# Kernel optimization log

Measured on AMD Instinct MI355X. Metric: run time of the kernel, lower is better.

## Reference

```python
import jax, jax.numpy as jnp
import numpy as np

B, S, DM = 2, 2048, 2048
H, DH = 16, 128
EPS = 1e-6


def rmsnorm(t, w):
    # normalize over last dim (head_dim), fp32 math
    var = jnp.mean(jnp.square(t), axis=-1, keepdims=True)
    return t * jax.lax.rsqrt(var + EPS) * w


def apply_rope(t, freqs):
    # t: (B,S,H,D); freqs: (S,1,D/2,2,2)
    b, s, h, d = t.shape
    t2 = t.reshape(b, s, h, 2, d // 2)
    t2 = jnp.moveaxis(t2, -2, -1)[..., None, :]  # (B,S,H,D/2,1,2)
    out = freqs[..., 0] * t2[..., 0] + freqs[..., 1] * t2[..., 1]  # (B,S,H,D/2,2)
    out = jnp.moveaxis(out, -1, -2).reshape(b, s, h, d)
    return out.astype(t.dtype)


def setup_inputs() -> dict:
    key = jax.random.key(0)
    ks = jax.random.split(key, 6)
    sc = 0.02
    return {
        "x": jax.random.normal(ks[0], (B, S, DM), jnp.float32),
        "rope_emb": jax.random.normal(ks[1], (S, 1, DH // 2, 2, 2), jnp.float32),
        "wq": jax.random.normal(ks[2], (DM, DM), jnp.float32) * sc,
        "wk": jax.random.normal(ks[3], (DM, DM), jnp.float32) * sc,
        "wv": jax.random.normal(ks[4], (DM, DM), jnp.float32) * sc,
        "wo": jax.random.normal(ks[5], (DM, DM), jnp.float32) * sc,
        "q_norm_w": jnp.ones((DH,), jnp.float32),
        "k_norm_w": jnp.ones((DH,), jnp.float32),
    }


def reference(x, rope_emb, wq, wk, wv, wo, q_norm_w, k_norm_w):
    b, s, _ = x.shape
    q = (x @ wq.T).reshape(b, s, H, DH)
    k = (x @ wk.T).reshape(b, s, H, DH)
    v = (x @ wv.T).reshape(b, s, H, DH)
    q = rmsnorm(q, q_norm_w)
    k = rmsnorm(k, k_norm_w)
    q = apply_rope(q, rope_emb)
    k = apply_rope(k, rope_emb)
    scale = 1.0 / np.sqrt(DH).astype(np.float32)
    scores = jnp.einsum('bqhd,bkhd->bhqk', q, k) * scale
    attn = jax.nn.softmax(scores, axis=-1)
    out = jnp.einsum('bhqk,bkhd->bqhd', attn, v).reshape(b, s, H * DH)
    return out @ wo.T
```

## Files before the change

kernel.cpp:

```cpp
#include <hip/hip_runtime.h>

typedef __bf16 bf16x8 __attribute__((ext_vector_type(8)));
typedef __bf16 bf16x4 __attribute__((ext_vector_type(4)));
typedef float floatx4 __attribute__((ext_vector_type(4)));

#define GK 2048
#define S_LEN 2048
#define NH 16
#define DH 128
#define NKT (GK / 64)

__device__ __forceinline__ void gl2lds16c(const __bf16* g, char* l) {
    __builtin_amdgcn_global_load_lds(
        (const __attribute__((address_space(1))) void*)g,
        (__attribute__((address_space(3))) void*)l, 16, 0, 0);
}

__global__ __launch_bounds__(256) void cvt_bf16(const float* __restrict__ in,
                                                __bf16* __restrict__ out, int n4) {
    int i = blockIdx.x * 256 + threadIdx.x;
    if (i < n4) {
        const float4 v = ((const float4*)in)[i];
        bf16x4 h;
        h[0] = (__bf16)v.x; h[1] = (__bf16)v.y; h[2] = (__bf16)v.z; h[3] = (__bf16)v.w;
        ((bf16x4*)out)[i] = h;
    }
}

__global__ __launch_bounds__(256) void cvt3_bf16(const float* __restrict__ a,
                                                 const float* __restrict__ b,
                                                 const float* __restrict__ c,
                                                 __bf16* __restrict__ out) {
    const int per = 2048 * 2048 / 4;
    int i = blockIdx.x * 256 + threadIdx.x;
    const float* src = a; int j = i;
    if (i >= 2 * per)      { src = c; j = i - 2 * per; }
    else if (i >= per)     { src = b; j = i - per; }
    const float4 v = ((const float4*)src)[j];
    bf16x4 h;
    h[0] = (__bf16)v.x; h[1] = (__bf16)v.y; h[2] = (__bf16)v.z; h[3] = (__bf16)v.w;
    ((bf16x4*)out)[i] = h;
}

__device__ __forceinline__ int xcd_remap(int L, int nwg) {
    return (L & 7) * (nwg >> 3) + (L >> 3);
}

__device__ __forceinline__ void gemm_body3(const __bf16* __restrict__ A,
                                           const __bf16* __restrict__ W,
                                           int m0, int n0, char* lds,
                                           floatx4 (*acc)[4]) {
    const int t = threadIdx.x, l = t & 63, wave = t >> 6;
    const int fr = l & 15, fq = l >> 4;
    const int wm = wave >> 2, wn = wave & 3;

    const int swcol = ((l & 7) * 8) ^ (((l >> 3) & 7) * 8);
    const __bf16* gA = A + (size_t)(m0 + wave * 8 + (l >> 3)) * GK + swcol;
    const __bf16* gW = W + (size_t)(n0 + wave * 8 + (l >> 3)) * GK + swcol;
    char* const ldsW = lds + wave * 1024;

    auto stageA = [&](int p, int kt, int q) {
        gl2lds16c(gA + (size_t)q * 64 * GK + kt * 64,
                  ldsW + p * 65536 + q * 8192);
    };
    auto stageBh = [&](int p, int kt, int h) {
        gl2lds16c(gW + (size_t)h * 64 * GK + kt * 64,
                  ldsW + p * 65536 + 32768 + h * 8192);
    };

#pragma unroll
    for (int q = 0; q < 4; q++) stageA(0, 0, q);
#pragma unroll
    for (int h = 0; h < 4; h++) stageBh(0, 0, h);
#pragma unroll
    for (int q = 0; q < 4; q++) stageA(1, 1, q);
#pragma unroll
    for (int h = 0; h < 4; h++) stageBh(1, 1, h);

    const int sw = (fr & 7) << 4;
    const int cb0 = (fq * 16) ^ sw;
    const int cb1 = (64 + fq * 16) ^ sw;

    for (int t0 = 0; t0 < NKT; t0++) {
        const int p = t0 & 1;
        if (t0 == NKT - 1) { asm volatile("s_waitcnt vmcnt(0)" ::: "memory"); }
        else               { asm volatile("s_waitcnt vmcnt(8)" ::: "memory"); }
        __builtin_amdgcn_s_barrier();
        asm volatile("" ::: "memory");

        const char* bufA = lds + p * 65536;
        const char* bufB = bufA + 32768;

        bf16x8 bB[4][2];
#pragma unroll
        for (int j = 0; j < 4; j++) {
            const char* rb = bufB + (wn * 64 + j * 16 + fr) * 128;
            bB[j][0] = *(const bf16x8*)(rb + cb0);
            bB[j][1] = *(const bf16x8*)(rb + cb1);
        }

#pragma unroll
        for (int q = 0; q < 4; q++) {
            if (t0 + 2 < NKT) {
                if (q == 1) { stageA(p, t0 + 2, 0); stageBh(p, t0 + 2, 0); stageBh(p, t0 + 2, 1); }
                if (q == 2) { stageA(p, t0 + 2, 1); stageBh(p, t0 + 2, 2); stageBh(p, t0 + 2, 3); }
                if (q == 3) { stageA(p, t0 + 2, 2); }
            }
            const char* ra = bufA + (q * 64 + wm * 32 + fr) * 128;
            bf16x8 bA[2][2];
#pragma unroll
            for (int i = 0; i < 2; i++) {
                bA[i][0] = *(const bf16x8*)(ra + i * 2048 + cb0);
                bA[i][1] = *(const bf16x8*)(ra + i * 2048 + cb1);
            }
            __builtin_amdgcn_s_setprio(1);
#pragma unroll
            for (int i = 0; i < 2; i++)
#pragma unroll
                for (int j = 0; j < 4; j++) {
                    acc[2 * q + i][j] = __builtin_amdgcn_mfma_f32_16x16x32_bf16(bA[i][0], bB[j][0], acc[2 * q + i][j], 0, 0, 0);
                    acc[2 * q + i][j] = __builtin_amdgcn_mfma_f32_16x16x32_bf16(bA[i][1], bB[j][1], acc[2 * q + i][j], 0, 0, 0);
                }
            __builtin_amdgcn_s_setprio(0);
            __builtin_amdgcn_s_barrier();
            asm volatile("" ::: "memory");
        }
        if (t0 + 2 < NKT) stageA(p, t0 + 2, 3);
    }
}

__global__ __launch_bounds__(512, 2) void gemm_qkv(const __bf16* __restrict__ A,
                                                   const __bf16* __restrict__ W,
                                                   __bf16* __restrict__ qb,
                                                   __bf16* __restrict__ kb,
                                                   __bf16* __restrict__ vbT) {
    extern __shared__ __align__(16) char lds[];
    const int gx = gridDim.x;
    const int L = blockIdx.x + gx * blockIdx.y;
    const int tid2 = xcd_remap(L, gx * (int)gridDim.y);
    const int m0 = (tid2 / gx) * 256, n0 = (tid2 % gx) * 256;
    floatx4 acc[8][4] = {};
    gemm_body3(A, W, m0, n0, lds, acc);

    const int lane = threadIdx.x & 63, wave = threadIdx.x >> 6;
    const int fr = lane & 15, fq = lane >> 4;
    const int wm = wave >> 2, wn = wave & 3;
    const int which = n0 >> 11;
    const int nc0 = n0 & 2047;

    for (int mi = 0; mi < 8; mi++)
        for (int j = 0; j < 4; j++) {
            const int row = m0 + (mi >> 1) * 64 + wm * 32 + (mi & 1) * 16 + fq * 4;
            const int col = nc0 + wn * 64 + j * 16 + fr;
            if (which == 2) {
                __bf16* Cp = vbT + (((size_t)(row & ~2047)) << 11) +
                             (size_t)col * 2048 + (row & 2047);
                bf16x4 hv;
                for (int r = 0; r < 4; r++) hv[r] = (__bf16)acc[mi][j][r];
                *(bf16x4*)Cp = hv;
            } else {
                __bf16* dst = which ? kb : qb;
                for (int r = 0; r < 4; r++)
                    dst[(size_t)(row + r) * 2048 + col] = (__bf16)acc[mi][j][r];
            }
        }
}

__global__ __launch_bounds__(512, 2) void gemm_out(const __bf16* __restrict__ A,
                                                   const __bf16* __restrict__ W,
                                                   float* __restrict__ C) {
    extern __shared__ __align__(16) char lds[];
    const int gx = gridDim.x;
    const int L = blockIdx.x + gx * blockIdx.y;
    const int tid2 = xcd_remap(L, gx * (int)gridDim.y);
    const int m0 = (tid2 / gx) * 256, n0 = (tid2 % gx) * 256;
    floatx4 acc[8][4] = {};
    gemm_body3(A, W, m0, n0, lds, acc);

    const int lane = threadIdx.x & 63, wave = threadIdx.x >> 6;
    const int fr = lane & 15, fq = lane >> 4;
    const int wm = wave >> 2, wn = wave & 3;
    for (int mi = 0; mi < 8; mi++)
        for (int j = 0; j < 4; j++) {
            const int row = m0 + (mi >> 1) * 64 + wm * 32 + (mi & 1) * 16 + fq * 4;
            const int col = n0 + wn * 64 + j * 16 + fr;
            for (int r = 0; r < 4; r++)
                C[(size_t)(row + r) * 2048 + col] = acc[mi][j][r];
        }
}

__global__ __launch_bounds__(256) void rmsrope(__bf16* __restrict__ qb,
                                               __bf16* __restrict__ kb,
                                               const float* __restrict__ rope,
                                               const float* __restrict__ qw,
                                               const float* __restrict__ kw) {
    const int lane = threadIdx.x & 63;
    const int row = blockIdx.x * 4 + (threadIdx.x >> 6);
    __bf16* p = (blockIdx.y ? kb : qb) + (size_t)row * DH;
    const float* w = blockIdx.y ? kw : qw;
    const int s = (row >> 4) & (S_LEN - 1);

    float t0 = (float)p[lane];
    float t1 = (float)p[lane + 64];
    float ss = t0 * t0 + t1 * t1;
    for (int o = 32; o; o >>= 1) ss += __shfl_xor(ss, o, 64);
    const float inv = rsqrtf(ss * (1.0f / 128.0f) + 1e-6f);
    t0 *= inv * w[lane];
    t1 *= inv * w[lane + 64];

    const float4 f = *(const float4*)(rope + (size_t)s * 256 + lane * 4);
    p[lane]      = (__bf16)(f.x * t0 + f.y * t1);
    p[lane + 64] = (__bf16)(f.z * t0 + f.w * t1);
}

__global__ __launch_bounds__(256, 2) void flash(const __bf16* __restrict__ Q,
                                                const __bf16* __restrict__ K,
                                                const __bf16* __restrict__ Vt_g,
                                                __bf16* __restrict__ O) {
    extern __shared__ __align__(16) char lds[];

    const int t = threadIdx.x, lane = t & 63, wave = t >> 6;
    const int fr = lane & 15, fq = lane >> 4;

    const int n = blockIdx.x + (int)gridDim.x * blockIdx.y;
    const int by = (n & 7) * 4 + (n >> 7);
    const int bx = (n >> 3) & 15;
    const int b = by >> 4, h = by & 15;

    const size_t baseQ = (size_t)b * S_LEN * 2048 + h * 128;
    const size_t baseV = (size_t)b * 2048 * 2048 + (size_t)h * 128 * 2048;
    const int q0 = bx * 128 + wave * 32;
    const float sc2 = 0.08838834764831845f * 1.4426950408889634f;
    const float M2 = 12.0f * 1.4426950408889634f;

    bf16x8 qf[2][4];
#pragma unroll
    for (int i2 = 0; i2 < 2; i2++) {
        const __bf16* qp = Q + baseQ + (size_t)(q0 + i2 * 16 + fr) * 2048 + fq * 8;
#pragma unroll
        for (int c = 0; c < 4; c++) qf[i2][c] = *(const bf16x8*)(qp + c * 32);
    }
    asm volatile("s_waitcnt vmcnt(0)" ::: "memory");

    bf16x8 onesb;
#pragma unroll
    for (int e = 0; e < 8; e++) onesb[e] = (__bf16)1.0f;

    const int l4 = lane >> 4;
    const int c16 = lane & 15;
    const int l3 = lane >> 3;
    const int c8 = lane & 7;
    const __bf16* gK0 = K + baseQ + (size_t)(wave * 16 + l4) * 2048 + (c16 ^ l4) * 8;
    const __bf16* gK1 = K + baseQ + (size_t)(wave * 16 + l4) * 2048 + (c16 ^ (4 + l4)) * 8;
    const __bf16* gV  = Vt_g + baseV + (size_t)(wave * 8 + l3) * 2048 + (c8 ^ l3) * 8;

    char* const kdw = lds + wave * 4096;
    char* const vdw = lds + 32768 + wave * 1024;

    auto stage = [&](int p, int it2) {
        const size_t ko = (size_t)it2 * 64 * 2048;
        char* kd = kdw + p * 16384;
        gl2lds16c(gK0 + ko,                      kd);
        gl2lds16c(gK1 + ko + (size_t)4 * 2048,   kd + 1024);
        gl2lds16c(gK0 + ko + (size_t)8 * 2048,   kd + 2048);
        gl2lds16c(gK1 + ko + (size_t)12 * 2048,  kd + 3072);
        const __bf16* v = gV + it2 * 64;
        char* vd = vdw + p * 16384;
        gl2lds16c(v,                        vd);
        gl2lds16c(v + (size_t)32 * 2048,    vd + 4096);
        gl2lds16c(v + (size_t)64 * 2048,    vd + 8192);
        gl2lds16c(v + (size_t)96 * 2048,    vd + 12288);
    };

    stage(0, 0);
    stage(1, 1);

    floatx4 oa[2][9] = {};
    char* const Pw = lds + 65536 + wave * 4096;
    const int sw = (fr & 7) << 4;

    for (int it = 0; it < 32; ++it) {
        const int p = it & 1;
        if (it == 31) { asm volatile("s_waitcnt vmcnt(0)" ::: "memory"); }
        else          { asm volatile("s_waitcnt vmcnt(8)" ::: "memory"); }
        __builtin_amdgcn_s_barrier();
        asm volatile("" ::: "memory");

        const char* Kb = lds + p * 16384;
        const char* Vb = lds + 32768 + p * 16384;

        floatx4 sacc[2][4] = {};
#pragma unroll
        for (int j = 0; j < 4; j++) {
            const char* kr = Kb + (j * 16 + fr) * 256;
            const bf16x8 kf0 = *(const bf16x8*)(kr + ((0 + fq * 16) ^ sw));
            const bf16x8 kf1 = *(const bf16x8*)(kr + ((64 + fq * 16) ^ sw));
            const bf16x8 kf2 = *(const bf16x8*)(kr + ((128 + fq * 16) ^ sw));
            const bf16x8 kf3 = *(const bf16x8*)(kr + ((192 + fq * 16) ^ sw));
            __builtin_amdgcn_s_setprio(1);
            sacc[0][j] = __builtin_amdgcn_mfma_f32_16x16x32_bf16(qf[0][0], kf0, sacc[0][j], 0, 0, 0);
            sacc[1][j] = __builtin_amdgcn_mfma_f32_16x16x32_bf16(qf[1][0], kf0, sacc[1][j], 0, 0, 0);
            sacc[0][j] = __builtin_amdgcn_mfma_f32_16x16x32_bf16(qf[0][1], kf1, sacc[0][j], 0, 0, 0);
            sacc[1][j] = __builtin_amdgcn_mfma_f32_16x16x32_bf16(qf[1][1], kf1, sacc[1][j], 0, 0, 0);
            sacc[0][j] = __builtin_amdgcn_mfma_f32_16x16x32_bf16(qf[0][2], kf2, sacc[0][j], 0, 0, 0);
            sacc[1][j] = __builtin_amdgcn_mfma_f32_16x16x32_bf16(qf[1][2], kf2, sacc[1][j], 0, 0, 0);
            sacc[0][j] = __builtin_amdgcn_mfma_f32_16x16x32_bf16(qf[0][3], kf3, sacc[0][j], 0, 0, 0);
            sacc[1][j] = __builtin_amdgcn_mfma_f32_16x16x32_bf16(qf[1][3], kf3, sacc[1][j], 0, 0, 0);
            __builtin_amdgcn_s_setprio(0);
        }

#pragma unroll
        for (int i2 = 0; i2 < 2; i2++)
#pragma unroll
            for (int r = 0; r < 4; r++) {
                const int row = i2 * 16 + fq * 4 + r;
                char* pr = Pw + row * 128;
                const int rsw = ((fq * 4 + r) & 7) << 4;
#pragma unroll
                for (int j = 0; j < 4; j++)
                    *(__bf16*)(pr + ((j * 32 + fr * 2) ^ rsw)) =
                        (__bf16)exp2f(fmaf(sc2, sacc[i2][j][r], -M2));
            }

        bf16x8 pf[2][2];
#pragma unroll
        for (int i2 = 0; i2 < 2; i2++) {
            const char* pr = Pw + (i2 * 16 + fr) * 128;
            pf[i2][0] = *(const bf16x8*)(pr + ((fq * 16) ^ sw));
            pf[i2][1] = *(const bf16x8*)(pr + ((64 + fq * 16) ^ sw));
        }
#pragma unroll
        for (int nb = 0; nb < 8; nb++) {
            const char* vr = Vb + (nb * 16 + fr) * 128;
            const bf16x8 vf0 = *(const bf16x8*)(vr + ((fq * 16) ^ sw));
            const bf16x8 vf1 = *(const bf16x8*)(vr + ((64 + fq * 16) ^ sw));
            __builtin_amdgcn_s_setprio(1);
            oa[0][nb] = __builtin_amdgcn_mfma_f32_16x16x32_bf16(pf[0][0], vf0, oa[0][nb], 0, 0, 0);
            oa[1][nb] = __builtin_amdgcn_mfma_f32_16x16x32_bf16(pf[1][0], vf0, oa[1][nb], 0, 0, 0);
            oa[0][nb] = __builtin_amdgcn_mfma_f32_16x16x32_bf16(pf[0][1], vf1, oa[0][nb], 0, 0, 0);
            oa[1][nb] = __builtin_amdgcn_mfma_f32_16x16x32_bf16(pf[1][1], vf1, oa[1][nb], 0, 0, 0);
            __builtin_amdgcn_s_setprio(0);
        }
        oa[0][8] = __builtin_amdgcn_mfma_f32_16x16x32_bf16(pf[0][0], onesb, oa[0][8], 0, 0, 0);
        oa[1][8] = __builtin_amdgcn_mfma_f32_16x16x32_bf16(pf[1][0], onesb, oa[1][8], 0, 0, 0);
        oa[0][8] = __builtin_amdgcn_mfma_f32_16x16x32_bf16(pf[0][1], onesb, oa[0][8], 0, 0, 0);
        oa[1][8] = __builtin_amdgcn_mfma_f32_16x16x32_bf16(pf[1][1], onesb, oa[1][8], 0, 0, 0);

        __builtin_amdgcn_s_barrier();
        asm volatile("" ::: "memory");
        if (it < 30) stage(p, it + 2);
    }

    for (int i2 = 0; i2 < 2; i2++)
        for (int r = 0; r < 4; r++) {
            const float inv = 1.0f / oa[i2][8][r];
            __bf16* op = O + baseQ + (size_t)(q0 + i2 * 16 + fq * 4 + r) * 2048;
            for (int nb = 0; nb < 8; nb++)
                op[nb * 16 + fr] = (__bf16)(oa[i2][nb][r] * inv);
        }
}

extern "C" void kernel_launch(void* const* d_in, const int* in_sizes, int n_in,
                              void* d_out, int out_size, void* d_ws, size_t ws_size,
                              hipStream_t stream) {
    const float* x    = (const float*)d_in[0];
    const float* rope = (const float*)d_in[1];
    const float* wq   = (const float*)d_in[2];
    const float* wk   = (const float*)d_in[3];
    const float* wv   = (const float*)d_in[4];
    const float* wo   = (const float*)d_in[5];
    const float* qnw  = (const float*)d_in[6];
    const float* knw  = (const float*)d_in[7];
    float* out = (float*)d_out;

    static bool attr_set = false;
    if (!attr_set) {
        hipFuncSetAttribute((const void*)gemm_qkv,
                            hipFuncAttributeMaxDynamicSharedMemorySize, 131072);
        hipFuncSetAttribute((const void*)gemm_out,
                            hipFuncAttributeMaxDynamicSharedMemorySize, 131072);
        hipFuncSetAttribute((const void*)flash,
                            hipFuncAttributeMaxDynamicSharedMemorySize, 81920);
        attr_set = true;
    }

    const size_t NTOK = 2 * 2048;
    const size_t ELEMS = NTOK * 2048;
    __bf16* xb  = (__bf16*)d_ws;
    __bf16* qb  = xb + ELEMS;
    __bf16* kb  = qb + ELEMS;
    __bf16* vbT = kb + ELEMS;
    __bf16* ob  = xb;
    __bf16* wqkv = (__bf16*)d_out;
    __bf16* wob  = qb;

    cvt_bf16<<<(int)(ELEMS / 4) / 256, 256, 0, stream>>>(x, xb, (int)(ELEMS / 4));
    cvt3_bf16<<<3 * (2048 * 2048 / 4) / 256, 256, 0, stream>>>(wq, wk, wv, wqkv);
    gemm_qkv<<<dim3(6144 / 256, (unsigned)(NTOK / 256)), 512, 131072, stream>>>(xb, wqkv, qb, kb, vbT);
    rmsrope<<<dim3((unsigned)(NTOK * 16 / 4), 2), 256, 0, stream>>>(qb, kb, rope, qnw, knw);
    flash<<<dim3(S_LEN / 128, 2 * 16), 256, 81920, stream>>>(qb, kb, vbT, ob);
    cvt_bf16<<<(int)(2048 * 2048 / 4) / 256, 256, 0, stream>>>(wo, wob, 2048 * 2048 / 4);
    gemm_out<<<dim3(2048 / 256, (unsigned)(NTOK / 256)), 512, 131072, stream>>>(ob, wob, out);
}
```

Before: 411.2 us.

## Shrink GEMM M-tile to 128 and double-buffer A fragments in registers

Both GEMMs now use 128x256 tiles instead of 256x256. This halves the A-stage LDS footprint (96KB instead of 128KB) and the accumulator registers, and doubles the grid size. The fix is meant for poor wave/CU fill: the out-projection launched only 128 blocks and the QKV GEMM 384 blocks. The inner loop prefetches the next A fragment from LDS before issuing the current MFMAs, and the async-copy schedule and wait counts are adjusted to match. The cost is lower arithmetic intensity per tile and more global traffic for the W operand.

After: 406.6 us. About the same (-1.1%).

```diff
diff --git a/kernel.cpp b/kernel.cpp
--- a/kernel.cpp
+++ b/kernel.cpp
@@ -46,7 +46,7 @@
     return (L & 7) * (nwg >> 3) + (L >> 3);
 }
 
-__device__ __forceinline__ void gemm_body3(const __bf16* __restrict__ A,
+__device__ __forceinline__ void gemm_body4(const __bf16* __restrict__ A,
                                            const __bf16* __restrict__ W,
                                            int m0, int n0, char* lds,
                                            floatx4 (*acc)[4]) {
@@ -59,21 +59,19 @@
     const __bf16* gW = W + (size_t)(n0 + wave * 8 + (l >> 3)) * GK + swcol;
     char* const ldsW = lds + wave * 1024;
 
-    auto stageA = [&](int p, int kt, int q) {
-        gl2lds16c(gA + (size_t)q * 64 * GK + kt * 64,
-                  ldsW + p * 65536 + q * 8192);
+    auto stageA = [&](int p, int kt, int c) {
+        gl2lds16c(gA + (size_t)c * 64 * GK + kt * 64,
+                  ldsW + p * 49152 + c * 8192);
     };
     auto stageBh = [&](int p, int kt, int h) {
         gl2lds16c(gW + (size_t)h * 64 * GK + kt * 64,
-                  ldsW + p * 65536 + 32768 + h * 8192);
+                  ldsW + p * 49152 + 16384 + h * 8192);
     };
 
-#pragma unroll
-    for (int q = 0; q < 4; q++) stageA(0, 0, q);
+    stageA(0, 0, 0); stageA(0, 0, 1);
 #pragma unroll
     for (int h = 0; h < 4; h++) stageBh(0, 0, h);
-#pragma unroll
-    for (int q = 0; q < 4; q++) stageA(1, 1, q);
+    stageA(1, 1, 0); stageA(1, 1, 1);
 #pragma unroll
     for (int h = 0; h < 4; h++) stageBh(1, 1, h);
 
@@ -84,12 +82,12 @@
     for (int t0 = 0; t0 < NKT; t0++) {
         const int p = t0 & 1;
         if (t0 == NKT - 1) { asm volatile("s_waitcnt vmcnt(0)" ::: "memory"); }
-        else               { asm volatile("s_waitcnt vmcnt(8)" ::: "memory"); }
+        else               { asm volatile("s_waitcnt vmcnt(6)" ::: "memory"); }
         __builtin_amdgcn_s_barrier();
         asm volatile("" ::: "memory");
 
-        const char* bufA = lds + p * 65536;
-        const char* bufB = bufA + 32768;
+        const char* bufA = lds + p * 49152;
+        const char* bufB = bufA + 16384;
 
         bf16x8 bB[4][2];
 #pragma unroll
@@ -98,34 +96,35 @@
             bB[j][0] = *(const bf16x8*)(rb + cb0);
             bB[j][1] = *(const bf16x8*)(rb + cb1);
         }
+        bf16x8 af[2][2];
+        {
+            const char* ra = bufA + (wm * 16 + fr) * 128;
+            af[0][0] = *(const bf16x8*)(ra + cb0);
+            af[0][1] = *(const bf16x8*)(ra + cb1);
+        }
 
 #pragma unroll
         for (int q = 0; q < 4; q++) {
             if (t0 + 2 < NKT) {
-                if (q == 1) { stageA(p, t0 + 2, 0); stageBh(p, t0 + 2, 0); stageBh(p, t0 + 2, 1); }
-                if (q == 2) { stageA(p, t0 + 2, 1); stageBh(p, t0 + 2, 2); stageBh(p, t0 + 2, 3); }
-                if (q == 3) { stageA(p, t0 + 2, 2); }
+                if (q == 1) { stageBh(p, t0 + 2, 0); stageBh(p, t0 + 2, 1); }
+                if (q == 2) { stageBh(p, t0 + 2, 2); stageBh(p, t0 + 2, 3); stageA(p, t0 + 2, 0); }
             }
-            const char* ra = bufA + (q * 64 + wm * 32 + fr) * 128;
-            bf16x8 bA[2][2];
-#pragma unroll
-            for (int i = 0; i < 2; i++) {
-                bA[i][0] = *(const bf16x8*)(ra + i * 2048 + cb0);
-                bA[i][1] = *(const bf16x8*)(ra + i * 2048 + cb1);
+            if (q < 3) {
+                const char* ra = bufA + ((q + 1) * 32 + wm * 16 + fr) * 128;
+                af[(q + 1) & 1][0] = *(const bf16x8*)(ra + cb0);
+                af[(q + 1) & 1][1] = *(const bf16x8*)(ra + cb1);
             }
             __builtin_amdgcn_s_setprio(1);
 #pragma unroll
-            for (int i = 0; i < 2; i++)
-#pragma unroll
-                for (int j = 0; j < 4; j++) {
-                    acc[2 * q + i][j] = __builtin_amdgcn_mfma_f32_16x16x32_bf16(bA[i][0], bB[j][0], acc[2 * q + i][j], 0, 0, 0);
-                    acc[2 * q + i][j] = __builtin_amdgcn_mfma_f32_16x16x32_bf16(bA[i][1], bB[j][1], acc[2 * q + i][j], 0, 0, 0);
-                }
+            for (int j = 0; j < 4; j++) {
+                acc[q][j] = __builtin_amdgcn_mfma_f32_16x16x32_bf16(af[q & 1][0], bB[j][0], acc[q][j], 0, 0, 0);
+                acc[q][j] = __builtin_amdgcn_mfma_f32_16x16x32_bf16(af[q & 1][1], bB[j][1], acc[q][j], 0, 0, 0);
+            }
             __builtin_amdgcn_s_setprio(0);
             __builtin_amdgcn_s_barrier();
             asm volatile("" ::: "memory");
         }
-        if (t0 + 2 < NKT) stageA(p, t0 + 2, 3);
+        if (t0 + 2 < NKT) stageA(p, t0 + 2, 1);
     }
 }
 
@@ -138,9 +137,9 @@
     const int gx = gridDim.x;
     const int L = blockIdx.x + gx * blockIdx.y;
     const int tid2 = xcd_remap(L, gx * (int)gridDim.y);
-    const int m0 = (tid2 / gx) * 256, n0 = (tid2 % gx) * 256;
-    floatx4 acc[8][4] = {};
-    gemm_body3(A, W, m0, n0, lds, acc);
+    const int m0 = (tid2 / gx) * 128, n0 = (tid2 % gx) * 256;
+    floatx4 acc[4][4] = {};
+    gemm_body4(A, W, m0, n0, lds, acc);
 
     const int lane = threadIdx.x & 63, wave = threadIdx.x >> 6;
     const int fr = lane & 15, fq = lane >> 4;
@@ -148,9 +147,9 @@
     const int which = n0 >> 11;
     const int nc0 = n0 & 2047;
 
-    for (int mi = 0; mi < 8; mi++)
+    for (int mi = 0; mi < 4; mi++)
         for (int j = 0; j < 4; j++) {
-            const int row = m0 + (mi >> 1) * 64 + wm * 32 + (mi & 1) * 16 + fq * 4;
+            const int row = m0 + mi * 32 + wm * 16 + fq * 4;
             const int col = nc0 + wn * 64 + j * 16 + fr;
             if (which == 2) {
                 __bf16* Cp = vbT + (((size_t)(row & ~2047)) << 11) +
@@ -173,16 +172,16 @@
     const int gx = gridDim.x;
     const int L = blockIdx.x + gx * blockIdx.y;
     const int tid2 = xcd_remap(L, gx * (int)gridDim.y);
-    const int m0 = (tid2 / gx) * 256, n0 = (tid2 % gx) * 256;
-    floatx4 acc[8][4] = {};
-    gemm_body3(A, W, m0, n0, lds, acc);
+    const int m0 = (tid2 / gx) * 128, n0 = (tid2 % gx) * 256;
+    floatx4 acc[4][4] = {};
+    gemm_body4(A, W, m0, n0, lds, acc);
 
     const int lane = threadIdx.x & 63, wave = threadIdx.x >> 6;
     const int fr = lane & 15, fq = lane >> 4;
     const int wm = wave >> 2, wn = wave & 3;
-    for (int mi = 0; mi < 8; mi++)
+    for (int mi = 0; mi < 4; mi++)
         for (int j = 0; j < 4; j++) {
-            const int row = m0 + (mi >> 1) * 64 + wm * 32 + (mi & 1) * 16 + fq * 4;
+            const int row = m0 + mi * 32 + wm * 16 + fq * 4;
             const int col = n0 + wn * 64 + j * 16 + fr;
             for (int r = 0; r < 4; r++)
                 C[(size_t)(row + r) * 2048 + col] = acc[mi][j][r];
@@ -376,9 +375,9 @@
     static bool attr_set = false;
     if (!attr_set) {
         hipFuncSetAttribute((const void*)gemm_qkv,
-                            hipFuncAttributeMaxDynamicSharedMemorySize, 131072);
+                            hipFuncAttributeMaxDynamicSharedMemorySize, 98304);
         hipFuncSetAttribute((const void*)gemm_out,
-                            hipFuncAttributeMaxDynamicSharedMemorySize, 131072);
+                            hipFuncAttributeMaxDynamicSharedMemorySize, 98304);
         hipFuncSetAttribute((const void*)flash,
                             hipFuncAttributeMaxDynamicSharedMemorySize, 81920);
         attr_set = true;
@@ -396,9 +395,9 @@
 
     cvt_bf16<<<(int)(ELEMS / 4) / 256, 256, 0, stream>>>(x, xb, (int)(ELEMS / 4));
     cvt3_bf16<<<3 * (2048 * 2048 / 4) / 256, 256, 0, stream>>>(wq, wk, wv, wqkv);
-    gemm_qkv<<<dim3(6144 / 256, (unsigned)(NTOK / 256)), 512, 131072, stream>>>(xb, wqkv, qb, kb, vbT);
+    gemm_qkv<<<dim3(6144 / 256, (unsigned)(NTOK / 128)), 512, 98304, stream>>>(xb, wqkv, qb, kb, vbT);
     rmsrope<<<dim3((unsigned)(NTOK * 16 / 4), 2), 256, 0, stream>>>(qb, kb, rope, qnw, knw);
     flash<<<dim3(S_LEN / 128, 2 * 16), 256, 81920, stream>>>(qb, kb, vbT, ob);
     cvt_bf16<<<(int)(2048 * 2048 / 4) / 256, 256, 0, stream>>>(wo, wob, 2048 * 2048 / 4);
-    gemm_out<<<dim3(2048 / 256, (unsigned)(NTOK / 256)), 512, 131072, stream>>>(ob, wob, out);
-}
+    gemm_out<<<dim3(2048 / 256, (unsigned)(NTOK / 128)), 512, 98304, stream>>>(ob, wob, out);
+}
```
